# Performance work log

Hardware: AMD Instinct MI355X
Metric: run time of the kernel (lower is better)

## Reference

```python
import jax, jax.numpy as jnp
import numpy as np


def setup_inputs() -> dict:
    key = jax.random.key(0)
    ks = jax.random.split(key, 6)
    B, N1, N2 = 4, 16384, 4096
    C1, C2 = 128, 256
    H1, H2 = 256, 128
    Cin = C1 + C2  # 384
    return {
        "xyz1": jax.random.normal(ks[0], (B, N1, 3), dtype=jnp.float32),
        "xyz2": jax.random.normal(ks[1], (B, N2, 3), dtype=jnp.float32),
        "features1": jax.random.normal(ks[2], (B, N1, C1), dtype=jnp.float32),
        "features2": jax.random.normal(ks[3], (B, N2, C2), dtype=jnp.float32),
        "W1": jax.random.normal(ks[4], (Cin, H1), dtype=jnp.float32) * (1.0 / np.sqrt(Cin)),
        "b1": jnp.zeros((H1,), dtype=jnp.float32),
        "W2": jax.random.normal(ks[5], (H1, H2), dtype=jnp.float32) * (1.0 / np.sqrt(H1)),
        "b2": jnp.zeros((H2,), dtype=jnp.float32),
    }


def reference(xyz1, xyz2, features1, features2, W1, b1, W2, b2):
    # Pairwise squared distances: [B, N1, N2]
    diff = xyz1[:, :, None, :] - xyz2[:, None, :, :]
    dist = jnp.sum(diff * diff, axis=-1)
    # 3 smallest distances (tf.argsort ascending, take first 3)
    neg_d3, idx = jax.lax.top_k(-dist, 3)          # idx: [B, N1, 3]
    d3 = jnp.maximum(-neg_d3, 1e-10)
    w = 1.0 / d3
    w = w / jnp.sum(w, axis=-1, keepdims=True)      # [B, N1, 3]
    # Gather features2 at the 3-NN indices per batch: [B, N1, 3, C2]
    gathered = jax.vmap(lambda f, i: f[i])(features2, idx)
    interp = jnp.sum(gathered * w[..., None], axis=2)  # [B, N1, C2]
    new_features = jnp.concatenate([interp, features1], axis=-1)  # [B, N1, C1+C2]
    # Pointwise MLP (Dense + ReLU, no BN)
    h = jax.nn.relu(jnp.einsum("bnc,ch->bnh", new_features, W1) + b1)
    out = jax.nn.relu(jnp.einsum("bnh,ho->bno", h, W2) + b2)
    return out
```

## Files before the change

### kernel.cpp

```cpp
#include <hip/hip_runtime.h>
#include <hip/hip_bf16.h>

typedef __bf16 bf16_t;
typedef __attribute__((ext_vector_type(8))) __bf16 bf16x8;
typedef __attribute__((ext_vector_type(4))) __bf16 bf16x4;
typedef __attribute__((ext_vector_type(4))) float f32x4;

#define N1 16384
#define N2 4096
#define C1 128
#define C2 256
#define CIN 384
#define HD1 256
#define HD2 128
#define BDIM 4
#define CHUNK 512
#define NCHUNK 8
#define NCAND 24

__global__ void prep_w(const float* __restrict__ W1, const float* __restrict__ W2,
                       bf16_t* __restrict__ W1t, bf16_t* __restrict__ W2t) {
  int tid = blockIdx.x * 256 + threadIdx.x;
  if (tid < CIN * HD1) {
    int k = tid / HD1, n = tid % HD1;
    W1t[n * CIN + k] = (bf16_t)W1[tid];
  }
  if (tid < HD1 * HD2) {
    int k = tid / HD2, n = tid % HD2;
    W2t[n * HD1 + k] = (bf16_t)W2[tid];
  }
}

__global__ __launch_bounds__(256) void knn_chunk(
    const float* __restrict__ xyz1, const float* __restrict__ xyz2,
    float* __restrict__ candd, int* __restrict__ candj) {
  int b  = blockIdx.y;
  int ck = blockIdx.z;
  int i  = blockIdx.x * 256 + threadIdx.x;
  const float* p = xyz1 + ((size_t)b * N1 + i) * 3;
  float px = p[0], py = p[1], pz = p[2];

  const float* x2b = xyz2 + ((size_t)b * N2 + (size_t)ck * CHUNK) * 3;

  float d0 = 3.4e38f, d1 = 3.4e38f, d2 = 3.4e38f;
  int   j0 = 0, j1 = 0, j2 = 0;

  for (int j = 0; j < CHUNK; j += 16) {
    float c[48];
    const float4* q = (const float4*)(x2b + 3 * j);
#pragma unroll
    for (int t = 0; t < 12; ++t) {
      float4 v = q[t];
      c[4 * t + 0] = v.x; c[4 * t + 1] = v.y; c[4 * t + 2] = v.z; c[4 * t + 3] = v.w;
    }
#pragma unroll
    for (int u = 0; u < 16; ++u) {
      float dx = __fsub_rn(c[3 * u + 0], px);
      float dy = __fsub_rn(c[3 * u + 1], py);
      float dz = __fsub_rn(c[3 * u + 2], pz);
      float d = __fadd_rn(__fadd_rn(__fmul_rn(dx, dx), __fmul_rn(dy, dy)),
                          __fmul_rn(dz, dz));
      int jj = j + u;
      if (d < d2) {
        bool lt0 = d < d0, lt1 = d < d1;
        j2 = lt1 ? j1 : jj;
        j1 = lt0 ? j0 : (lt1 ? jj : j1);
        j0 = lt0 ? jj : j0;
        d2 = __builtin_amdgcn_fmed3f(d, d1, d2);
        d1 = __builtin_amdgcn_fmed3f(d, d0, d1);
        d0 = fminf(d, d0);
      }
    }
  }
  size_t qb = ((size_t)b * N1 + i) * NCAND + (size_t)ck * 3;
  int jbase = ck * CHUNK;
  candd[qb + 0] = d0; candd[qb + 1] = d1; candd[qb + 2] = d2;
  candj[qb + 0] = j0 + jbase; candj[qb + 1] = j1 + jbase; candj[qb + 2] = j2 + jbase;
}

__global__ __launch_bounds__(256) void knn_merge(
    const float* __restrict__ candd, const int* __restrict__ candj,
    float* __restrict__ wq, int* __restrict__ iq) {
  int q = blockIdx.x * 256 + threadIdx.x;
  const float* cd = candd + (size_t)q * NCAND;
  const int*   cj = candj + (size_t)q * NCAND;
  float d0 = 3.4e38f, d1 = 3.4e38f, d2 = 3.4e38f;
  int   j0 = 0, j1 = 0, j2 = 0;
#pragma unroll
  for (int c = 0; c < NCAND; ++c) {
    float d = cd[c]; int j = cj[c];
    bool p0 = d < d0, p1 = d < d1, p2 = d < d2;
    j2 = p1 ? j1 : (p2 ? j : j2);
    j1 = p0 ? j0 : (p1 ? j : j1);
    j0 = p0 ? j : j0;
    d2 = __builtin_amdgcn_fmed3f(d, d1, d2);
    d1 = __builtin_amdgcn_fmed3f(d, d0, d1);
    d0 = fminf(d, d0);
  }
  d0 = fmaxf(d0, 1e-10f); d1 = fmaxf(d1, 1e-10f); d2 = fmaxf(d2, 1e-10f);
  float w0 = 1.0f / d0, w1 = 1.0f / d1, w2 = 1.0f / d2;
  float ws = w0 + w1 + w2;
  wq[q * 3 + 0] = w0 / ws; wq[q * 3 + 1] = w1 / ws; wq[q * 3 + 2] = w2 / ws;
  iq[q * 3 + 0] = j0; iq[q * 3 + 1] = j1; iq[q * 3 + 2] = j2;
}

__global__ __launch_bounds__(256, 2) void interp_gemm1(
    const float* __restrict__ f1, const float* __restrict__ f2,
    const float* __restrict__ wq, const int* __restrict__ iq,
    const bf16_t* __restrict__ W1t, const float* __restrict__ b1,
    bf16_t* __restrict__ Hbuf) {
  __shared__ __align__(16) bf16_t As[128 * 32];
  __shared__ __align__(16) bf16_t Bs[4 * 256 * 8];
  int tid  = threadIdx.x;
  int wv   = tid >> 6, ln = tid & 63;
  int quad = ln >> 4, lm = ln & 15;
  long row0 = (long)blockIdx.x * 128;

  int srow = tid >> 1;
  int sh   = tid & 1;
  long q = row0 + srow;
  int  b = (int)(q >> 14);
  float u0 = wq[q * 3 + 0], u1 = wq[q * 3 + 1], u2 = wq[q * 3 + 2];
  const float* f2b = f2 + (size_t)b * N2 * C2;
  const float* r0 = f2b + (size_t)iq[q * 3 + 0] * C2;
  const float* r1 = f2b + (size_t)iq[q * 3 + 1] * C2;
  const float* r2 = f2b + (size_t)iq[q * 3 + 2] * C2;
  const float* f1r = f1 + (size_t)q * C1;
  bf16_t* asd = As + srow * 32 + sh * 16;

  int wm = (wv >> 1) * 64, wn = (wv & 1) * 128;
  f32x4 acc[4][8] = {};

  for (int ks = 0; ks < 12; ++ks) {
    int kb = ks * 32;
#pragma unroll
    for (int s = 0; s < 4; ++s) {
      __builtin_amdgcn_global_load_lds(
          (const __attribute__((address_space(1))) void*)(
              W1t + (size_t)(wv * 64 + ln) * CIN + kb + s * 8),
          (__attribute__((address_space(3))) void*)(Bs + s * 2048 + wv * 512),
          16, 0, 0);
    }
    bf16x8 o[2];
    if (ks < 8) {
      int cb = kb + sh * 16;
#pragma unroll
      for (int c4 = 0; c4 < 4; ++c4) {
        float4 v0 = *(const float4*)(r0 + cb + c4 * 4);
        float4 v1 = *(const float4*)(r1 + cb + c4 * 4);
        float4 v2 = *(const float4*)(r2 + cb + c4 * 4);
        int oi = c4 >> 1, off = (c4 & 1) * 4;
        o[oi][off + 0] = (bf16_t)(u0 * v0.x + u1 * v1.x + u2 * v2.x);
        o[oi][off + 1] = (bf16_t)(u0 * v0.y + u1 * v1.y + u2 * v2.y);
        o[oi][off + 2] = (bf16_t)(u0 * v0.z + u1 * v1.z + u2 * v2.z);
        o[oi][off + 3] = (bf16_t)(u0 * v0.w + u1 * v1.w + u2 * v2.w);
      }
    } else {
      int cf = kb - 256 + sh * 16;
#pragma unroll
      for (int c4 = 0; c4 < 4; ++c4) {
        float4 g = *(const float4*)(f1r + cf + c4 * 4);
        int oi = c4 >> 1, off = (c4 & 1) * 4;
        o[oi][off + 0] = (bf16_t)g.x;
        o[oi][off + 1] = (bf16_t)g.y;
        o[oi][off + 2] = (bf16_t)g.z;
        o[oi][off + 3] = (bf16_t)g.w;
      }
    }
    *(bf16x8*)(asd) = o[0];
    *(bf16x8*)(asd + 8) = o[1];
    __syncthreads();

    bf16x8 af[4];
#pragma unroll
    for (int mi = 0; mi < 4; ++mi)
      af[mi] = *(const bf16x8*)(As + (wm + mi * 16 + lm) * 32 + quad * 8);
#pragma unroll
    for (int nh = 0; nh < 2; ++nh) {
      bf16x8 bfr[4];
#pragma unroll
      for (int nn = 0; nn < 4; ++nn)
        bfr[nn] = *(const bf16x8*)(Bs + quad * 2048 + (wn + (nh * 4 + nn) * 16 + lm) * 8);
#pragma unroll
      for (int mi = 0; mi < 4; ++mi)
#pragma unroll
        for (int nn = 0; nn < 4; ++nn)
          acc[mi][nh * 4 + nn] = __builtin_amdgcn_mfma_f32_16x16x32_bf16(
              af[mi], bfr[nn], acc[mi][nh * 4 + nn], 0, 0, 0);
    }
    __syncthreads();
  }

#pragma unroll
  for (int mi = 0; mi < 4; ++mi)
#pragma unroll
    for (int ni = 0; ni < 8; ++ni) {
      int col = wn + ni * 16 + lm;
      float bv = b1[col];
#pragma unroll
      for (int r = 0; r < 4; ++r) {
        long rowg = row0 + wm + mi * 16 + quad * 4 + r;
        float v = acc[mi][ni][r] + bv;
        v = fmaxf(v, 0.0f);
        Hbuf[rowg * HD1 + col] = (bf16_t)v;
      }
    }
}

template <bool OUT_BF16>
__global__ __launch_bounds__(256) void gemm_bt(
    const bf16_t* __restrict__ A, const bf16_t* __restrict__ Bt,
    const float* __restrict__ bias, void* __restrict__ Cout,
    int M, int N, int K) {
  __shared__ __align__(16) bf16_t As[128 * 32];
  __shared__ __align__(16) bf16_t Bs[128 * 32];
  int tid  = threadIdx.x;
  int wv   = tid >> 6, ln = tid & 63;
  int quad = ln >> 4, lm = ln & 15;
  long row0 = (long)blockIdx.x * 128;
  int  col0 = blockIdx.y * 128;
  const bf16_t* Ab = A + row0 * K;
  const bf16_t* Bb = Bt + (long)col0 * K;
  f32x4 acc[4][4] = {};
  int wm = (wv >> 1) * 64, wn = (wv & 1) * 64;

  for (int k0 = 0; k0 < K; k0 += 32) {
#pragma unroll
    for (int t = 0; t < 2; ++t) {
      int c = t * 256 + tid;
      int r = c >> 2, kc = (c & 3) << 3;
      __builtin_amdgcn_global_load_lds(
          (const __attribute__((address_space(1))) void*)(Ab + (long)r * K + k0 + kc),
          (__attribute__((address_space(3))) void*)(As + (t * 256 + wv * 64) * 8),
          16, 0, 0);
      __builtin_amdgcn_global_load_lds(
          (const __attribute__((address_space(1))) void*)(Bb + (long)r * K + k0 + kc),
          (__attribute__((address_space(3))) void*)(Bs + (t * 256 + wv * 64) * 8),
          16, 0, 0);
    }
    __syncthreads();
    bf16x8 af[4], bfr[4];
#pragma unroll
    for (int mi = 0; mi < 4; ++mi)
      af[mi] = *(const bf16x8*)(As + (wm + mi * 16 + lm) * 32 + quad * 8);
#pragma unroll
    for (int ni = 0; ni < 4; ++ni)
      bfr[ni] = *(const bf16x8*)(Bs + (wn + ni * 16 + lm) * 32 + quad * 8);
#pragma unroll
    for (int mi = 0; mi < 4; ++mi)
#pragma unroll
      for (int ni = 0; ni < 4; ++ni)
        acc[mi][ni] = __builtin_amdgcn_mfma_f32_16x16x32_bf16(af[mi], bfr[ni],
                                                              acc[mi][ni], 0, 0, 0);
    __syncthreads();
  }

#pragma unroll
  for (int mi = 0; mi < 4; ++mi)
#pragma unroll
    for (int ni = 0; ni < 4; ++ni) {
      int col = col0 + wn + ni * 16 + lm;
      float bv = bias[col];
#pragma unroll
      for (int r = 0; r < 4; ++r) {
        long rowg = row0 + wm + mi * 16 + quad * 4 + r;
        float v = acc[mi][ni][r] + bv;
        v = fmaxf(v, 0.0f);
        if (OUT_BF16) ((bf16_t*)Cout)[rowg * N + col] = (bf16_t)v;
        else          ((float*)Cout)[rowg * N + col]  = v;
      }
    }
}

extern "C" void kernel_launch(void* const* d_in, const int* in_sizes, int n_in,
                              void* d_out, int out_size, void* d_ws, size_t ws_size,
                              hipStream_t stream) {
  const float* xyz1 = (const float*)d_in[0];
  const float* xyz2 = (const float*)d_in[1];
  const float* f1   = (const float*)d_in[2];
  const float* f2   = (const float*)d_in[3];
  const float* W1   = (const float*)d_in[4];
  const float* b1   = (const float*)d_in[5];
  const float* W2   = (const float*)d_in[6];
  const float* b2   = (const float*)d_in[7];
  float* out = (float*)d_out;

  const size_t NQ = (size_t)BDIM * N1;
  char* ws = (char*)d_ws;
  bf16_t* W1t = (bf16_t*)ws;
  bf16_t* W2t = (bf16_t*)(ws + (256 << 10));
  float*  wq  = (float*)(ws + (512 << 10));
  int*    iq  = (int*)(ws + (1536 << 10));
  char*   hb  = ws + (2560 << 10) + NQ * CIN * 2;
  bf16_t* Hbuf  = (bf16_t*)hb;
  float*  candd = (float*)hb;
  int*    candj = (int*)(hb + NQ * NCAND * 4);

  prep_w<<<dim3(384), dim3(256), 0, stream>>>(W1, W2, W1t, W2t);
  knn_chunk<<<dim3(N1 / 256, BDIM, NCHUNK), dim3(256), 0, stream>>>(
      xyz1, xyz2, candd, candj);
  knn_merge<<<dim3(NQ / 256), dim3(256), 0, stream>>>(candd, candj, wq, iq);
  interp_gemm1<<<dim3(NQ / 128), dim3(256), 0, stream>>>(
      f1, f2, wq, iq, W1t, b1, Hbuf);
  gemm_bt<false><<<dim3(NQ / 128, HD2 / 128), dim3(256), 0, stream>>>(
      Hbuf, W2t, b2, (void*)out, NQ, HD2, HD1);
}
```

Before: 256.4 us.

## Fuse KNN into one pass with expanded-distance prefilter against running threshold

Replaces the chunked KNN kernel and its separate merge kernel with one kernel that scans all N2 candidates per query. It precomputes |y|^2 next to xyz2 in a float4 table. A cheap 3-FMA expanded-distance test then rejects candidates that cannot beat the current third-best, and only the survivors get the exact distance and insertion. The goal is less arithmetic per candidate, no candidate buffer round-trip through memory, and one fewer launch. In exchange the grid drops to 256 blocks, which lowers occupancy and latency hiding, and a wave still takes the slow path whenever any lane passes the filter.

```diff
diff --git a/kernel.cpp b/kernel.cpp
--- a/kernel.cpp
+++ b/kernel.cpp
@@ -14,12 +14,11 @@
 #define HD1 256
 #define HD2 128
 #define BDIM 4
-#define CHUNK 512
-#define NCHUNK 8
-#define NCAND 24
 
 __global__ void prep_w(const float* __restrict__ W1, const float* __restrict__ W2,
-                       bf16_t* __restrict__ W1t, bf16_t* __restrict__ W2t) {
+                       const float* __restrict__ xyz2,
+                       bf16_t* __restrict__ W1t, bf16_t* __restrict__ W2t,
+                       float4* __restrict__ xyzr) {
   int tid = blockIdx.x * 256 + threadIdx.x;
   if (tid < CIN * HD1) {
     int k = tid / HD1, n = tid % HD1;
@@ -29,77 +28,75 @@
     int k = tid / HD2, n = tid % HD2;
     W2t[n * HD1 + k] = (bf16_t)W2[tid];
   }
-}
-
-__global__ __launch_bounds__(256) void knn_chunk(
-    const float* __restrict__ xyz1, const float* __restrict__ xyz2,
-    float* __restrict__ candd, int* __restrict__ candj) {
-  int b  = blockIdx.y;
-  int ck = blockIdx.z;
-  int i  = blockIdx.x * 256 + threadIdx.x;
+  if (tid < BDIM * N2) {
+    const float* s = xyz2 + (size_t)tid * 3;
+    float x = s[0], y = s[1], z = s[2];
+    float4 v; v.x = x; v.y = y; v.z = z; v.w = x * x + y * y + z * z;
+    xyzr[tid] = v;
+  }
+}
+
+__global__ __launch_bounds__(256) void knn2(
+    const float* __restrict__ xyz1, const float4* __restrict__ xyzr,
+    float* __restrict__ wq, int* __restrict__ iq) {
+  int b = blockIdx.y;
+  int i = blockIdx.x * 256 + threadIdx.x;
   const float* p = xyz1 + ((size_t)b * N1 + i) * 3;
   float px = p[0], py = p[1], pz = p[2];
-
-  const float* x2b = xyz2 + ((size_t)b * N2 + (size_t)ck * CHUNK) * 3;
+  float qx = -2.0f * px, qy = -2.0f * py, qz = -2.0f * pz;
+  float r1 = px * px + py * py + pz * pz;
+  const float4* base = xyzr + (size_t)b * N2;
 
   float d0 = 3.4e38f, d1 = 3.4e38f, d2 = 3.4e38f;
   int   j0 = 0, j1 = 0, j2 = 0;
-
-  for (int j = 0; j < CHUNK; j += 16) {
-    float c[48];
-    const float4* q = (const float4*)(x2b + 3 * j);
-#pragma unroll
-    for (int t = 0; t < 12; ++t) {
-      float4 v = q[t];
-      c[4 * t + 0] = v.x; c[4 * t + 1] = v.y; c[4 * t + 2] = v.z; c[4 * t + 3] = v.w;
-    }
-#pragma unroll
-    for (int u = 0; u < 16; ++u) {
-      float dx = __fsub_rn(c[3 * u + 0], px);
-      float dy = __fsub_rn(c[3 * u + 1], py);
-      float dz = __fsub_rn(c[3 * u + 2], pz);
-      float d = __fadd_rn(__fadd_rn(__fmul_rn(dx, dx), __fmul_rn(dy, dy)),
-                          __fmul_rn(dz, dz));
-      int jj = j + u;
-      if (d < d2) {
-        bool lt0 = d < d0, lt1 = d < d1;
-        j2 = lt1 ? j1 : jj;
-        j1 = lt0 ? j0 : (lt1 ? jj : j1);
-        j0 = lt0 ? jj : j0;
-        d2 = __builtin_amdgcn_fmed3f(d, d1, d2);
-        d1 = __builtin_amdgcn_fmed3f(d, d0, d1);
-        d0 = fminf(d, d0);
-      }
-    }
-  }
-  size_t qb = ((size_t)b * N1 + i) * NCAND + (size_t)ck * 3;
-  int jbase = ck * CHUNK;
-  candd[qb + 0] = d0; candd[qb + 1] = d1; candd[qb + 2] = d2;
-  candj[qb + 0] = j0 + jbase; candj[qb + 1] = j1 + jbase; candj[qb + 2] = j2 + jbase;
-}
-
-__global__ __launch_bounds__(256) void knn_merge(
-    const float* __restrict__ candd, const int* __restrict__ candj,
-    float* __restrict__ wq, int* __restrict__ iq) {
-  int q = blockIdx.x * 256 + threadIdx.x;
-  const float* cd = candd + (size_t)q * NCAND;
-  const int*   cj = candj + (size_t)q * NCAND;
-  float d0 = 3.4e38f, d1 = 3.4e38f, d2 = 3.4e38f;
-  int   j0 = 0, j1 = 0, j2 = 0;
-#pragma unroll
-  for (int c = 0; c < NCAND; ++c) {
-    float d = cd[c]; int j = cj[c];
-    bool p0 = d < d0, p1 = d < d1, p2 = d < d2;
-    j2 = p1 ? j1 : (p2 ? j : j2);
-    j1 = p0 ? j0 : (p1 ? j : j1);
-    j0 = p0 ? j : j0;
-    d2 = __builtin_amdgcn_fmed3f(d, d1, d2);
-    d1 = __builtin_amdgcn_fmed3f(d, d0, d1);
-    d0 = fminf(d, d0);
-  }
+  float thr = 3.4e38f;
+
+  auto proc8 = [&](const float4* cb, int g) {
+#pragma unroll
+    for (int u = 0; u < 8; ++u) {
+      float4 c = cb[u];
+      float dt = __builtin_fmaf(qx, c.x, c.w);
+      dt = __builtin_fmaf(qy, c.y, dt);
+      dt = __builtin_fmaf(qz, c.z, dt);
+      if (dt <= thr) {
+        float dx = __fsub_rn(c.x, px);
+        float dy = __fsub_rn(c.y, py);
+        float dz = __fsub_rn(c.z, pz);
+        float d = __fadd_rn(__fadd_rn(__fmul_rn(dx, dx), __fmul_rn(dy, dy)),
+                            __fmul_rn(dz, dz));
+        int jj = g + u;
+        if (d < d2) {
+          bool lt0 = d < d0, lt1 = d < d1;
+          j2 = lt1 ? j1 : jj;
+          j1 = lt0 ? j0 : (lt1 ? jj : j1);
+          j0 = lt0 ? jj : j0;
+          d2 = __builtin_amdgcn_fmed3f(d, d1, d2);
+          d1 = __builtin_amdgcn_fmed3f(d, d0, d1);
+          d0 = fminf(d, d0);
+          thr = __fadd_rn(__fsub_rn(d2, r1), 1e-3f);
+        }
+      }
+    }
+  };
+
+  float4 A[8], Bv[8];
+#pragma unroll
+  for (int t = 0; t < 8; ++t) A[t] = base[t];
+#pragma unroll
+  for (int t = 0; t < 8; ++t) Bv[t] = base[8 + t];
+  for (int g = 0; g < N2; g += 16) {
+    proc8(A, g);
+#pragma unroll
+    for (int t = 0; t < 8; ++t) A[t] = base[g + 16 + t];
+    proc8(Bv, g + 8);
+#pragma unroll
+    for (int t = 0; t < 8; ++t) Bv[t] = base[g + 24 + t];
+  }
+
   d0 = fmaxf(d0, 1e-10f); d1 = fmaxf(d1, 1e-10f); d2 = fmaxf(d2, 1e-10f);
   float w0 = 1.0f / d0, w1 = 1.0f / d1, w2 = 1.0f / d2;
   float ws = w0 + w1 + w2;
+  size_t q = (size_t)b * N1 + i;
   wq[q * 3 + 0] = w0 / ws; wq[q * 3 + 1] = w1 / ws; wq[q * 3 + 2] = w2 / ws;
   iq[q * 3 + 0] = j0; iq[q * 3 + 1] = j1; iq[q * 3 + 2] = j2;
 }
@@ -291,15 +288,12 @@
   bf16_t* W2t = (bf16_t*)(ws + (256 << 10));
   float*  wq  = (float*)(ws + (512 << 10));
   int*    iq  = (int*)(ws + (1536 << 10));
+  float4* xyzr = (float4*)(ws + (2560 << 10));
   char*   hb  = ws + (2560 << 10) + NQ * CIN * 2;
   bf16_t* Hbuf  = (bf16_t*)hb;
-  float*  candd = (float*)hb;
-  int*    candj = (int*)(hb + NQ * NCAND * 4);
-
-  prep_w<<<dim3(384), dim3(256), 0, stream>>>(W1, W2, W1t, W2t);
-  knn_chunk<<<dim3(N1 / 256, BDIM, NCHUNK), dim3(256), 0, stream>>>(
-      xyz1, xyz2, candd, candj);
-  knn_merge<<<dim3(NQ / 256), dim3(256), 0, stream>>>(candd, candj, wq, iq);
+
+  prep_w<<<dim3(384), dim3(256), 0, stream>>>(W1, W2, xyz2, W1t, W2t, xyzr);
+  knn2<<<dim3(N1 / 256, BDIM), dim3(256), 0, stream>>>(xyz1, xyzr, wq, iq);
   interp_gemm1<<<dim3(NQ / 128), dim3(256), 0, stream>>>(
       f1, f2, wq, iq, W1t, b1, Hbuf);
   gemm_bt<false><<<dim3(NQ / 128, HD2 / 128), dim3(256), 0, stream>>>(
```

After: 367.5 us. +43.3%, slower.

## Prefilter KNN candidates with expanded-norm distance bound and pack xyz2 as float4

Applied to the files above, without the earlier changes.

The kernel precomputes xyz2 as float4 rows with the squared norm in w. The KNN scan first evaluates a cheap three-FMA distance surrogate (|c|^2 - 2p·c) and only computes the exact distance and updates the top-3 when it falls under a threshold taken from the current third-best distance. Chunks double in size and their count halves, which halves the candidate buffer and the merge work. In exchange there is more serial work per thread and fewer blocks, and the 1e-3 slack on the threshold affects how often the exact path is skipped.

```diff
diff --git a/kernel.cpp b/kernel.cpp
--- a/kernel.cpp
+++ b/kernel.cpp
@@ -14,12 +14,14 @@
 #define HD1 256
 #define HD2 128
 #define BDIM 4
-#define CHUNK 512
-#define NCHUNK 8
-#define NCAND 24
+#define CHUNK 1024
+#define NCHUNK 4
+#define NCAND 12
 
 __global__ void prep_w(const float* __restrict__ W1, const float* __restrict__ W2,
-                       bf16_t* __restrict__ W1t, bf16_t* __restrict__ W2t) {
+                       const float* __restrict__ xyz2,
+                       bf16_t* __restrict__ W1t, bf16_t* __restrict__ W2t,
+                       float4* __restrict__ xyzr) {
   int tid = blockIdx.x * 256 + threadIdx.x;
   if (tid < CIN * HD1) {
     int k = tid / HD1, n = tid % HD1;
@@ -29,46 +31,58 @@
     int k = tid / HD2, n = tid % HD2;
     W2t[n * HD1 + k] = (bf16_t)W2[tid];
   }
-}
-
-__global__ __launch_bounds__(256) void knn_chunk(
-    const float* __restrict__ xyz1, const float* __restrict__ xyz2,
+  if (tid < BDIM * N2) {
+    const float* s = xyz2 + (size_t)tid * 3;
+    float x = s[0], y = s[1], z = s[2];
+    float4 v; v.x = x; v.y = y; v.z = z; v.w = x * x + y * y + z * z;
+    xyzr[tid] = v;
+  }
+}
+
+__global__ __launch_bounds__(256) void knn_chunk3(
+    const float* __restrict__ xyz1, const float4* __restrict__ xyzr,
     float* __restrict__ candd, int* __restrict__ candj) {
   int b  = blockIdx.y;
   int ck = blockIdx.z;
   int i  = blockIdx.x * 256 + threadIdx.x;
   const float* p = xyz1 + ((size_t)b * N1 + i) * 3;
   float px = p[0], py = p[1], pz = p[2];
-
-  const float* x2b = xyz2 + ((size_t)b * N2 + (size_t)ck * CHUNK) * 3;
+  float qx = -2.0f * px, qy = -2.0f * py, qz = -2.0f * pz;
+  float r1 = px * px + py * py + pz * pz;
+
+  const float4* x2b = xyzr + (size_t)b * N2 + (size_t)ck * CHUNK;
 
   float d0 = 3.4e38f, d1 = 3.4e38f, d2 = 3.4e38f;
   int   j0 = 0, j1 = 0, j2 = 0;
+  float thr = 3.4e38f;
 
   for (int j = 0; j < CHUNK; j += 16) {
-    float c[48];
-    const float4* q = (const float4*)(x2b + 3 * j);
-#pragma unroll
-    for (int t = 0; t < 12; ++t) {
-      float4 v = q[t];
-      c[4 * t + 0] = v.x; c[4 * t + 1] = v.y; c[4 * t + 2] = v.z; c[4 * t + 3] = v.w;
-    }
+    float4 c4[16];
+#pragma unroll
+    for (int t = 0; t < 16; ++t) c4[t] = x2b[j + t];
 #pragma unroll
     for (int u = 0; u < 16; ++u) {
-      float dx = __fsub_rn(c[3 * u + 0], px);
-      float dy = __fsub_rn(c[3 * u + 1], py);
-      float dz = __fsub_rn(c[3 * u + 2], pz);
-      float d = __fadd_rn(__fadd_rn(__fmul_rn(dx, dx), __fmul_rn(dy, dy)),
-                          __fmul_rn(dz, dz));
-      int jj = j + u;
-      if (d < d2) {
-        bool lt0 = d < d0, lt1 = d < d1;
-        j2 = lt1 ? j1 : jj;
-        j1 = lt0 ? j0 : (lt1 ? jj : j1);
-        j0 = lt0 ? jj : j0;
-        d2 = __builtin_amdgcn_fmed3f(d, d1, d2);
-        d1 = __builtin_amdgcn_fmed3f(d, d0, d1);
-        d0 = fminf(d, d0);
+      float4 c = c4[u];
+      float dt = __builtin_fmaf(qz, c.z, c.w);
+      dt = __builtin_fmaf(qy, c.y, dt);
+      dt = __builtin_fmaf(qx, c.x, dt);
+      if (dt <= thr) {
+        float dx = __fsub_rn(c.x, px);
+        float dy = __fsub_rn(c.y, py);
+        float dz = __fsub_rn(c.z, pz);
+        float d = __fadd_rn(__fadd_rn(__fmul_rn(dx, dx), __fmul_rn(dy, dy)),
+                            __fmul_rn(dz, dz));
+        int jj = j + u;
+        if (d < d2) {
+          bool lt0 = d < d0, lt1 = d < d1;
+          j2 = lt1 ? j1 : jj;
+          j1 = lt0 ? j0 : (lt1 ? jj : j1);
+          j0 = lt0 ? jj : j0;
+          d2 = __builtin_amdgcn_fmed3f(d, d1, d2);
+          d1 = __builtin_amdgcn_fmed3f(d, d0, d1);
+          d0 = fminf(d, d0);
+          thr = __fadd_rn(__fsub_rn(d2, r1), 1e-3f);
+        }
       }
     }
   }
@@ -291,14 +305,15 @@
   bf16_t* W2t = (bf16_t*)(ws + (256 << 10));
   float*  wq  = (float*)(ws + (512 << 10));
   int*    iq  = (int*)(ws + (1536 << 10));
+  float4* xyzr = (float4*)(ws + (2560 << 10));
   char*   hb  = ws + (2560 << 10) + NQ * CIN * 2;
   bf16_t* Hbuf  = (bf16_t*)hb;
   float*  candd = (float*)hb;
   int*    candj = (int*)(hb + NQ * NCAND * 4);
 
-  prep_w<<<dim3(384), dim3(256), 0, stream>>>(W1, W2, W1t, W2t);
-  knn_chunk<<<dim3(N1 / 256, BDIM, NCHUNK), dim3(256), 0, stream>>>(
-      xyz1, xyz2, candd, candj);
+  prep_w<<<dim3(384), dim3(256), 0, stream>>>(W1, W2, xyz2, W1t, W2t, xyzr);
+  knn_chunk3<<<dim3(N1 / 256, BDIM, NCHUNK), dim3(256), 0, stream>>>(
+      xyz1, xyzr, candd, candj);
   knn_merge<<<dim3(NQ / 256), dim3(256), 0, stream>>>(candd, candj, wq, iq);
   interp_gemm1<<<dim3(NQ / 128), dim3(256), 0, stream>>>(
       f1, f2, wq, iq, W1t, b1, Hbuf);
```

After: 261.7 us. 1.02x slower.

## Pre-convert features2 to bf16 and prefetch gather rows one K-step ahead

Applied to the files above, without the earlier changes.

The prep kernel now also converts features2 to bf16 into workspace (2048 blocks cover all 4M elements). The interpolation+GEMM1 kernel then gathers bf16 neighbor rows, which halves the gather bytes. It also software-prefetches the next K-step's gathered rows and features1 values into registers after the barrier, so load latency overlaps the MFMA work. The costs are an extra full pass over features2 in prep_w and higher register pressure under launch_bounds(256,2).

```diff
diff --git a/kernel.cpp b/kernel.cpp
--- a/kernel.cpp
+++ b/kernel.cpp
@@ -19,7 +19,9 @@
 #define NCAND 24
 
 __global__ void prep_w(const float* __restrict__ W1, const float* __restrict__ W2,
-                       bf16_t* __restrict__ W1t, bf16_t* __restrict__ W2t) {
+                       const float* __restrict__ f2,
+                       bf16_t* __restrict__ W1t, bf16_t* __restrict__ W2t,
+                       bf16_t* __restrict__ f2bf) {
   int tid = blockIdx.x * 256 + threadIdx.x;
   if (tid < CIN * HD1) {
     int k = tid / HD1, n = tid % HD1;
@@ -29,6 +31,12 @@
     int k = tid / HD2, n = tid % HD2;
     W2t[n * HD1 + k] = (bf16_t)W2[tid];
   }
+  const float4* s4 = (const float4*)f2;
+  float4 a = s4[2 * (size_t)tid], b = s4[2 * (size_t)tid + 1];
+  bf16x8 o;
+  o[0] = (bf16_t)a.x; o[1] = (bf16_t)a.y; o[2] = (bf16_t)a.z; o[3] = (bf16_t)a.w;
+  o[4] = (bf16_t)b.x; o[5] = (bf16_t)b.y; o[6] = (bf16_t)b.z; o[7] = (bf16_t)b.w;
+  *(bf16x8*)(f2bf + (size_t)tid * 8) = o;
 }
 
 __global__ __launch_bounds__(256) void knn_chunk(
@@ -105,7 +113,7 @@
 }
 
 __global__ __launch_bounds__(256, 2) void interp_gemm1(
-    const float* __restrict__ f1, const float* __restrict__ f2,
+    const float* __restrict__ f1, const bf16_t* __restrict__ f2b_,
     const float* __restrict__ wq, const int* __restrict__ iq,
     const bf16_t* __restrict__ W1t, const float* __restrict__ b1,
     bf16_t* __restrict__ Hbuf) {
@@ -121,15 +129,24 @@
   long q = row0 + srow;
   int  b = (int)(q >> 14);
   float u0 = wq[q * 3 + 0], u1 = wq[q * 3 + 1], u2 = wq[q * 3 + 2];
-  const float* f2b = f2 + (size_t)b * N2 * C2;
-  const float* r0 = f2b + (size_t)iq[q * 3 + 0] * C2;
-  const float* r1 = f2b + (size_t)iq[q * 3 + 1] * C2;
-  const float* r2 = f2b + (size_t)iq[q * 3 + 2] * C2;
+  const bf16_t* f2bb = f2b_ + (size_t)b * N2 * C2;
+  const bf16_t* r0 = f2bb + (size_t)iq[q * 3 + 0] * C2;
+  const bf16_t* r1 = f2bb + (size_t)iq[q * 3 + 1] * C2;
+  const bf16_t* r2 = f2bb + (size_t)iq[q * 3 + 2] * C2;
   const float* f1r = f1 + (size_t)q * C1;
   bf16_t* asd = As + srow * 32 + sh * 16;
 
   int wm = (wv >> 1) * 64, wn = (wv & 1) * 128;
   f32x4 acc[4][8] = {};
+
+  bf16x8 g0a, g0b, g1a, g1b, g2a, g2b;
+  float4 gf[4];
+  {
+    int cb = sh * 16;
+    g0a = *(const bf16x8*)(r0 + cb); g0b = *(const bf16x8*)(r0 + cb + 8);
+    g1a = *(const bf16x8*)(r1 + cb); g1b = *(const bf16x8*)(r1 + cb + 8);
+    g2a = *(const bf16x8*)(r2 + cb); g2b = *(const bf16x8*)(r2 + cb + 8);
+  }
 
   for (int ks = 0; ks < 12; ++ks) {
     int kb = ks * 32;
@@ -143,23 +160,17 @@
     }
     bf16x8 o[2];
     if (ks < 8) {
-      int cb = kb + sh * 16;
+#pragma unroll
+      for (int e = 0; e < 8; ++e) {
+        o[0][e] = (bf16_t)(u0 * (float)g0a[e] + u1 * (float)g1a[e] +
+                           u2 * (float)g2a[e]);
+        o[1][e] = (bf16_t)(u0 * (float)g0b[e] + u1 * (float)g1b[e] +
+                           u2 * (float)g2b[e]);
+      }
+    } else {
 #pragma unroll
       for (int c4 = 0; c4 < 4; ++c4) {
-        float4 v0 = *(const float4*)(r0 + cb + c4 * 4);
-        float4 v1 = *(const float4*)(r1 + cb + c4 * 4);
-        float4 v2 = *(const float4*)(r2 + cb + c4 * 4);
-        int oi = c4 >> 1, off = (c4 & 1) * 4;
-        o[oi][off + 0] = (bf16_t)(u0 * v0.x + u1 * v1.x + u2 * v2.x);
-        o[oi][off + 1] = (bf16_t)(u0 * v0.y + u1 * v1.y + u2 * v2.y);
-        o[oi][off + 2] = (bf16_t)(u0 * v0.z + u1 * v1.z + u2 * v2.z);
-        o[oi][off + 3] = (bf16_t)(u0 * v0.w + u1 * v1.w + u2 * v2.w);
-      }
-    } else {
-      int cf = kb - 256 + sh * 16;
-#pragma unroll
-      for (int c4 = 0; c4 < 4; ++c4) {
-        float4 g = *(const float4*)(f1r + cf + c4 * 4);
+        float4 g = gf[c4];
         int oi = c4 >> 1, off = (c4 & 1) * 4;
         o[oi][off + 0] = (bf16_t)g.x;
         o[oi][off + 1] = (bf16_t)g.y;
@@ -170,6 +181,18 @@
     *(bf16x8*)(asd) = o[0];
     *(bf16x8*)(asd + 8) = o[1];
     __syncthreads();
+
+    if (ks < 7) {
+      int cb = (ks + 1) * 32 + sh * 16;
+      g0a = *(const bf16x8*)(r0 + cb); g0b = *(const bf16x8*)(r0 + cb + 8);
+      g1a = *(const bf16x8*)(r1 + cb); g1b = *(const bf16x8*)(r1 + cb + 8);
+      g2a = *(const bf16x8*)(r2 + cb); g2b = *(const bf16x8*)(r2 + cb + 8);
+    } else if (ks < 11) {
+      int cf = (ks - 7) * 32 + sh * 16;
+#pragma unroll
+      for (int c4 = 0; c4 < 4; ++c4)
+        gf[c4] = *(const float4*)(f1r + cf + c4 * 4);
+    }
 
     bf16x8 af[4];
 #pragma unroll
@@ -291,17 +314,18 @@
   bf16_t* W2t = (bf16_t*)(ws + (256 << 10));
   float*  wq  = (float*)(ws + (512 << 10));
   int*    iq  = (int*)(ws + (1536 << 10));
+  bf16_t* f2bf = (bf16_t*)(ws + (2560 << 10));
   char*   hb  = ws + (2560 << 10) + NQ * CIN * 2;
   bf16_t* Hbuf  = (bf16_t*)hb;
   float*  candd = (float*)hb;
   int*    candj = (int*)(hb + NQ * NCAND * 4);
 
-  prep_w<<<dim3(384), dim3(256), 0, stream>>>(W1, W2, W1t, W2t);
+  prep_w<<<dim3(2048), dim3(256), 0, stream>>>(W1, W2, f2, W1t, W2t, f2bf);
   knn_chunk<<<dim3(N1 / 256, BDIM, NCHUNK), dim3(256), 0, stream>>>(
       xyz1, xyz2, candd, candj);
   knn_merge<<<dim3(NQ / 256), dim3(256), 0, stream>>>(candd, candj, wq, iq);
   interp_gemm1<<<dim3(NQ / 128), dim3(256), 0, stream>>>(
-      f1, f2, wq, iq, W1t, b1, Hbuf);
+      f1, f2bf, wq, iq, W1t, b1, Hbuf);
   gemm_bt<false><<<dim3(NQ / 128, HD2 / 128), dim3(256), 0, stream>>>(
       Hbuf, W2t, b2, (void*)out, NQ, HD2, HD1);
 }
```

After: 245.0 us, median of 2. 4.4% less time.
